# Optimization experiments

Hardware: AMD Instinct MI355X
Metric: run time of the kernel (lower is better)

## Reference

```python
import jax, jax.numpy as jnp
import numpy as np
from jax.ops import segment_sum, segment_max

N_NODES = 50000
N_EDGES = 640000
N_GRAPHS = 128
IN_DIM = 128
HID = 128
OUT_DIM = 2


def setup_inputs() -> dict:
    key = jax.random.key(0)
    ks = jax.random.split(key, 16)
    x = jax.random.normal(ks[0], (N_NODES, IN_DIM), dtype=jnp.float32)
    edge_index = jax.random.randint(ks[1], (2, N_EDGES), 0, N_NODES, dtype=jnp.int64)
    batch = jnp.sort(jax.random.randint(ks[2], (N_NODES,), 0, N_GRAPHS, dtype=jnp.int64))
    s = 0.05
    return {
        "x": x,
        "edge_index": edge_index,
        "batch": batch,
        "w0": jax.random.normal(ks[3], (HID, IN_DIM), dtype=jnp.float32) * s,
        "b0": jnp.zeros((HID,), jnp.float32),
        "w1": jax.random.normal(ks[4], (HID, HID), dtype=jnp.float32) * s,
        "b1": jnp.zeros((HID,), jnp.float32),
        "w2": jax.random.normal(ks[5], (HID, HID), dtype=jnp.float32) * s,
        "b2": jnp.zeros((HID,), jnp.float32),
        "gate_w": jax.random.normal(ks[6], (1, HID), dtype=jnp.float32) * s,
        "gate_b": jnp.zeros((1,), jnp.float32),
        "lin_w": jax.random.normal(ks[7], (2 * HID, HID), dtype=jnp.float32) * s,
        "lin_b": jnp.zeros((2 * HID,), jnp.float32),
        "cls_w": jax.random.normal(ks[8], (OUT_DIM, 2 * HID), dtype=jnp.float32) * s,
        "cls_b": jnp.zeros((OUT_DIM,), jnp.float32),
    }


def _gcn_norm(edge_index, n):
    # add self loops, symmetric normalization D^-1/2 (A+I) D^-1/2
    loop = jnp.arange(n, dtype=edge_index.dtype)
    row = jnp.concatenate([edge_index[0], loop])
    col = jnp.concatenate([edge_index[1], loop])
    deg = segment_sum(jnp.ones_like(col, dtype=jnp.float32), col, num_segments=n)
    dis = jnp.where(deg > 0, jax.lax.rsqrt(deg), 0.0)
    norm = dis[row] * dis[col]
    return row, col, norm


def _gcn_conv(x, w, b, row, col, norm, n):
    xw = x @ w.T + b                     # [N, hid]
    msg = norm[:, None] * xw[row]        # gather + scale, [E+N, hid]
    return segment_sum(msg, col, num_segments=n)


def _att_pool(x, gate_w, gate_b, batch, g):
    gate = x @ gate_w.T + gate_b         # [N, 1]
    m = segment_max(gate, batch, num_segments=g)        # [G, 1]
    e = jnp.exp(gate - m[batch])
    s = segment_sum(e, batch, num_segments=g)           # [G, 1]
    alpha = e / s[batch]                                # [N, 1]
    return segment_sum(alpha * x, batch, num_segments=g)  # [G, hid]


def reference(x, edge_index, batch, w0, b0, w1, b1, w2, b2,
              gate_w, gate_b, lin_w, lin_b, cls_w, cls_b):
    n = N_NODES
    g = N_GRAPHS
    row, col, norm = _gcn_norm(edge_index, n)
    hg = None
    for w, b in ((w0, b0), (w1, b1), (w2, b2)):
        x = _gcn_conv(x, w, b, row, col, norm, n)
        x = jax.nn.relu(x)  # dropout is identity in eval mode
        pooled = _att_pool(x, gate_w, gate_b, batch, g)
        hg = pooled if hg is None else hg + pooled
    out = jax.nn.relu(hg @ lin_w.T + lin_b)
    return out @ cls_w.T + cls_b
```

## Files before the change

kernel.cpp:

```cpp
#include <hip/hip_runtime.h>
#include <hip/hip_bf16.h>
#include <float.h>

#define N_NODES  50000
#define N_EDGES  640000
#define N_GRAPHS 128
#define DIM      128
#define CAP      64
#define ZROW     N_NODES
#define NSLICE   8
#define SLICE_W  6250
#define NCHUNK   256
#define CHUNK_E  2500

typedef __attribute__((ext_vector_type(8))) short bf16x8;
typedef __attribute__((ext_vector_type(4))) float f32x4;

__device__ __forceinline__ unsigned short f2bf(float f){
  unsigned int u = __float_as_uint(f);
  u += 0x7fffu + ((u >> 16) & 1u);
  return (unsigned short)(u >> 16);
}
__device__ __forceinline__ float bf2f(unsigned short h){
  return __uint_as_float(((unsigned int)h) << 16);
}
__device__ __forceinline__ float2 up2(unsigned int p){
  return make_float2(__uint_as_float(p << 16),
                     __uint_as_float(p & 0xffff0000u));
}

__global__ __launch_bounds__(256) void zero_misc(int* __restrict__ cnt,
    unsigned int* __restrict__ z0, unsigned int* __restrict__ z1){
  int i = blockIdx.x*256 + threadIdx.x;
  if (i < N_NODES) cnt[i] = 0;
  else if (i < N_NODES + 64) z0[i - N_NODES] = 0;
  else if (i < N_NODES + 128) z1[i - N_NODES - 64] = 0;
}

__global__ __launch_bounds__(256) void scatter_sliced(
    const int* __restrict__ ei, int* __restrict__ cnt, int* __restrict__ srcb){
  int slice = blockIdx.x & (NSLICE-1);
  int chunk = blockIdx.x >> 3;
  int e0 = chunk * CHUNK_E;
  for (int e = e0 + threadIdx.x; e < e0 + CHUNK_E; e += 256){
    int c = ei[N_EDGES + e];
    if (c / SLICE_W == slice){
      int r = ei[e];
      int pos = atomicAdd(&cnt[c], 1);
      srcb[(c << 6) + pos] = r;
    }
  }
}

__global__ __launch_bounds__(256) void prep(
    const int* __restrict__ cnt, float* __restrict__ dis,
    const int* __restrict__ batch, int* __restrict__ gs,
    const float* __restrict__ w0, const float* __restrict__ w1,
    const float* __restrict__ w2, unsigned int* __restrict__ o0,
    unsigned int* __restrict__ o1, unsigned int* __restrict__ o2){
  int b = blockIdx.x, tid = threadIdx.x;
  if (b < 196){
    int i = b*256 + tid;
    if (i < N_NODES){
      dis[i] = 1.0f / sqrtf((float)(cnt[i] + 1));
      int bb = batch[i];
      int bp = (i == 0) ? -1 : batch[i-1];
      for (int g = bp + 1; g <= bb; ++g) gs[g] = i;
      if (i == N_NODES - 1)
        for (int g = bb + 1; g <= N_GRAPHS; ++g) gs[g] = N_NODES;
    }
  } else {
    int i = (b - 196)*256 + tid;
    if (i < 3*8192){
      int a = i >> 13, j = i & 8191;
      const float* src = (a == 0) ? w0 : (a == 1) ? w1 : w2;
      unsigned int* dst = (a == 0) ? o0 : (a == 1) ? o1 : o2;
      float2 v = ((const float2*)src)[j];
      dst[j] = (unsigned int)f2bf(v.x) | ((unsigned int)f2bf(v.y) << 16);
    }
  }
}

template<bool F32IN>
__global__ __launch_bounds__(256, 2) void gemm_mfma(
    const void* __restrict__ Ain, const unsigned short* __restrict__ Wb,
    const float* __restrict__ bias, const float* __restrict__ dis,
    unsigned short* __restrict__ C, int total_waves){
  int tid = threadIdx.x;
  int lane = tid & 63;
  int wid = blockIdx.x*4 + (tid >> 6);
  int l15 = lane & 15, l4 = lane >> 4;
  bf16x8 wf[8][4];
  #pragma unroll
  for (int ob = 0; ob < 8; ++ob)
    #pragma unroll
    for (int ks = 0; ks < 4; ++ks)
      wf[ob][ks] = *(const bf16x8*)&Wb[(ob*16 + l15)*128 + ks*32 + l4*8];
  float bv[8];
  #pragma unroll
  for (int ob = 0; ob < 8; ++ob) bv[ob] = bias[ob*16 + l15];

  for (int t = wid; t < N_NODES/16; t += total_waves){
    int row0 = t*16;
    bf16x8 af[4];
    #pragma unroll
    for (int ks = 0; ks < 4; ++ks){
      if constexpr (F32IN){
        const float* A = (const float*)Ain;
        const float4* ap = (const float4*)&A[(size_t)(row0 + l15)*128 + ks*32 + l4*8];
        float4 fa = ap[0], fb = ap[1];
        bf16x8 v;
        v[0]=(short)f2bf(fa.x); v[1]=(short)f2bf(fa.y);
        v[2]=(short)f2bf(fa.z); v[3]=(short)f2bf(fa.w);
        v[4]=(short)f2bf(fb.x); v[5]=(short)f2bf(fb.y);
        v[6]=(short)f2bf(fb.z); v[7]=(short)f2bf(fb.w);
        af[ks] = v;
      } else {
        const unsigned short* A = (const unsigned short*)Ain;
        af[ks] = *(const bf16x8*)&A[(size_t)(row0 + l15)*128 + ks*32 + l4*8];
      }
    }
    f32x4 acc[8];
    #pragma unroll
    for (int ob = 0; ob < 8; ++ob) acc[ob] = (f32x4){0.f,0.f,0.f,0.f};
    #pragma unroll
    for (int ks = 0; ks < 4; ++ks)
      #pragma unroll
      for (int ob = 0; ob < 8; ++ob)
        acc[ob] = __builtin_amdgcn_mfma_f32_16x16x32_bf16(af[ks], wf[ob][ks],
                                                          acc[ob], 0, 0, 0);
    float dv[4];
    #pragma unroll
    for (int r = 0; r < 4; ++r) dv[r] = dis[row0 + l4*4 + r];
    #pragma unroll
    for (int ob = 0; ob < 8; ++ob)
      #pragma unroll
      for (int r = 0; r < 4; ++r)
        C[(size_t)(row0 + l4*4 + r)*128 + ob*16 + l15] =
            f2bf((acc[ob][r] + bv[ob]) * dv[r]);
  }
}

__global__ __launch_bounds__(256) void aggregate_bf(
    const uint4* __restrict__ xw4,
    const int* __restrict__ cnt, const int* __restrict__ srcb,
    const float* __restrict__ dis,
    uint4* __restrict__ xout4, const float* __restrict__ gw,
    const float* __restrict__ gb, float* __restrict__ gate){
  int tid  = threadIdx.x;
  int lane = tid & 63;
  int wv   = tid >> 6;
  int quad = wv >> 1;
  int par  = wv & 1;
  int sub  = lane >> 4, l16 = lane & 15;
  int node = blockIdx.x*8 + quad*4 + sub;
  int   n  = cnt[node];
  int base = node << 6;
  float acc[8];
  if (par == 0){
    uint4 v = xw4[node*16 + l16];
    float2 a0 = up2(v.x), a1 = up2(v.y), a2 = up2(v.z), a3 = up2(v.w);
    acc[0]=a0.x; acc[1]=a0.y; acc[2]=a1.x; acc[3]=a1.y;
    acc[4]=a2.x; acc[5]=a2.y; acc[6]=a3.x; acc[7]=a3.y;
  } else {
    #pragma unroll
    for (int i = 0; i < 8; ++i) acc[i] = 0.f;
  }
  int nmax = n;
  nmax = max(nmax, __shfl_xor(nmax, 16, 64));
  nmax = max(nmax, __shfl_xor(nmax, 32, 64));
  for (int e = par*8; e < nmax; e += 16){
    int4 sa = *(const int4*)&srcb[base + e];
    int4 sb = *(const int4*)&srcb[base + e + 4];
    int r0 = (e   < n) ? sa.x : ZROW;
    int r1 = (e+1 < n) ? sa.y : ZROW;
    int r2 = (e+2 < n) ? sa.z : ZROW;
    int r3 = (e+3 < n) ? sa.w : ZROW;
    int r4 = (e+4 < n) ? sb.x : ZROW;
    int r5 = (e+5 < n) ? sb.y : ZROW;
    int r6 = (e+6 < n) ? sb.z : ZROW;
    int r7 = (e+7 < n) ? sb.w : ZROW;
    uint4 u0 = xw4[r0*16 + l16];
    uint4 u1 = xw4[r1*16 + l16];
    uint4 u2 = xw4[r2*16 + l16];
    uint4 u3 = xw4[r3*16 + l16];
    uint4 u4 = xw4[r4*16 + l16];
    uint4 u5 = xw4[r5*16 + l16];
    uint4 u6 = xw4[r6*16 + l16];
    uint4 u7 = xw4[r7*16 + l16];
    #define ACC8(U) { \
      float2 b0=up2(U.x), b1=up2(U.y), b2=up2(U.z), b3=up2(U.w); \
      acc[0]+=b0.x; acc[1]+=b0.y; acc[2]+=b1.x; acc[3]+=b1.y;    \
      acc[4]+=b2.x; acc[5]+=b2.y; acc[6]+=b3.x; acc[7]+=b3.y; }
    ACC8(u0) ACC8(u1) ACC8(u2) ACC8(u3)
    ACC8(u4) ACC8(u5) ACC8(u6) ACC8(u7)
    #undef ACC8
  }
  __shared__ float comb[2][64][9];
  if (par == 1){
    #pragma unroll
    for (int i = 0; i < 8; ++i) comb[quad][lane][i] = acc[i];
  }
  __syncthreads();
  if (par == 0){
    float d = dis[node];
    #pragma unroll
    for (int i = 0; i < 8; ++i)
      acc[i] = fmaxf(d*(acc[i] + comb[quad][lane][i]), 0.f);
    uint4 o;
    o.x = (unsigned int)f2bf(acc[0]) | ((unsigned int)f2bf(acc[1]) << 16);
    o.y = (unsigned int)f2bf(acc[2]) | ((unsigned int)f2bf(acc[3]) << 16);
    o.z = (unsigned int)f2bf(acc[4]) | ((unsigned int)f2bf(acc[5]) << 16);
    o.w = (unsigned int)f2bf(acc[6]) | ((unsigned int)f2bf(acc[7]) << 16);
    xout4[node*16 + l16] = o;
    const float4* gw4 = (const float4*)gw;
    float4 g0 = gw4[l16*2], g1 = gw4[l16*2 + 1];
    float p = acc[0]*g0.x + acc[1]*g0.y + acc[2]*g0.z + acc[3]*g0.w
            + acc[4]*g1.x + acc[5]*g1.y + acc[6]*g1.z + acc[7]*g1.w;
    p += __shfl_xor(p, 1, 64);
    p += __shfl_xor(p, 2, 64);
    p += __shfl_xor(p, 4, 64);
    p += __shfl_xor(p, 8, 64);
    if (l16 == 0) gate[node] = p + gb[0];
  }
}

__global__ __launch_bounds__(256) void gate_reduce(float* __restrict__ gate,
    const int* __restrict__ gs){
  int g = blockIdx.x, tid = threadIdx.x;
  int s = gs[g], e = gs[g+1];
  __shared__ float red[256];
  float m = -FLT_MAX;
  for (int i = s + tid; i < e; i += 256) m = fmaxf(m, gate[i]);
  red[tid] = m; __syncthreads();
  for (int st = 128; st > 0; st >>= 1){
    if (tid < st) red[tid] = fmaxf(red[tid], red[tid+st]);
    __syncthreads();
  }
  m = red[0]; __syncthreads();
  float p = 0.f;
  for (int i = s + tid; i < e; i += 256){
    float ev = __expf(gate[i] - m);
    gate[i] = ev;
    p += ev;
  }
  red[tid] = p; __syncthreads();
  for (int st = 128; st > 0; st >>= 1){
    if (tid < st) red[tid] += red[tid+st];
    __syncthreads();
  }
  float inv = (red[0] > 0.f) ? 1.0f/red[0] : 0.f;
  for (int i = s + tid; i < e; i += 256) gate[i] *= inv;
}

__global__ __launch_bounds__(256) void att_pool_part(
    const unsigned int* __restrict__ x, const float* __restrict__ alpha,
    const int* __restrict__ gs, float* __restrict__ hgp){
  int g = blockIdx.x >> 3, q = blockIdx.x & 7, tid = threadIdx.x;
  int s = gs[g], e = gs[g+1];
  int d2 = tid & 63, rg = tid >> 6;
  float ax = 0.f, ay = 0.f;
  for (int i = s + q*4 + rg; i < e; i += 32){
    float a = alpha[i];
    float2 u = up2(x[(size_t)i*64 + d2]);
    ax += a*u.x; ay += a*u.y;
  }
  __shared__ float2 red[4][64];
  red[rg][d2] = make_float2(ax, ay);
  __syncthreads();
  if (tid < 64){
    float2 r0 = red[0][tid], r1 = red[1][tid], r2 = red[2][tid], r3 = red[3][tid];
    hgp[(size_t)blockIdx.x*128 + 2*tid    ] = r0.x + r1.x + r2.x + r3.x;
    hgp[(size_t)blockIdx.x*128 + 2*tid + 1] = r0.y + r1.y + r2.y + r3.y;
  }
}

__global__ __launch_bounds__(256) void head(const float* __restrict__ hgp,
    const float* __restrict__ lw, const float* __restrict__ lb,
    const float* __restrict__ cw, const float* __restrict__ cb,
    float* __restrict__ out){
  int g = blockIdx.x, tid = threadIdx.x;
  __shared__ float h[128];
  __shared__ float t1[256];
  __shared__ float red[256];
  if (tid < 128){
    float hv = 0.f;
    #pragma unroll
    for (int L = 0; L < 3; ++L){
      const float* hb = hgp + (size_t)(L*8*N_GRAPHS + 8*g)*128;
      #pragma unroll
      for (int q = 0; q < 8; ++q) hv += hb[q*128 + tid];
    }
    h[tid] = hv;
  }
  __syncthreads();
  const float* wr = lw + tid*128;
  float a = 0.f;
  for (int k = 0; k < 128; ++k) a += h[k]*wr[k];
  a = fmaxf(a + lb[tid], 0.f);
  t1[tid] = a;
  __syncthreads();
  int o = tid >> 7, j = tid & 127;
  float p = t1[j]*cw[o*256 + j] + t1[j+128]*cw[o*256 + j + 128];
  red[tid] = p; __syncthreads();
  for (int st = 64; st > 0; st >>= 1){
    if (j < st) red[tid] += red[tid+st];
    __syncthreads();
  }
  if (j == 0) out[g*2 + o] = red[tid] + cb[o];
}

extern "C" void kernel_launch(void* const* d_in, const int* in_sizes, int n_in,
                              void* d_out, int out_size, void* d_ws, size_t ws_size,
                              hipStream_t stream){
  const float* x   = (const float*)d_in[0];
  const int*   ei  = (const int*)d_in[1];
  const int* batch = (const int*)d_in[2];
  const float* w0  = (const float*)d_in[3];
  const float* b0  = (const float*)d_in[4];
  const float* w1  = (const float*)d_in[5];
  const float* b1  = (const float*)d_in[6];
  const float* w2  = (const float*)d_in[7];
  const float* b2  = (const float*)d_in[8];
  const float* gw  = (const float*)d_in[9];
  const float* gb  = (const float*)d_in[10];
  const float* lw  = (const float*)d_in[11];
  const float* lb  = (const float*)d_in[12];
  const float* cw  = (const float*)d_in[13];
  const float* cb  = (const float*)d_in[14];
  float* out = (float*)d_out;
  (void)in_sizes; (void)n_in; (void)out_size; (void)ws_size;

  char* ws = (char*)d_ws;
  size_t off = 0;
  auto alloc = [&](size_t bytes)->char*{
    char* p = ws + off;
    off = (off + bytes + 255) & ~(size_t)255;
    return p;
  };
  float* dis    = (float*)alloc((size_t)N_NODES*4);
  unsigned int* xw   = (unsigned int*)alloc((size_t)(N_NODES+1)*64*4);
  unsigned int* xbuf = (unsigned int*)alloc((size_t)(N_NODES+1)*64*4);
  unsigned int* Wb0  = (unsigned int*)alloc((size_t)DIM*64*4);
  unsigned int* Wb1  = (unsigned int*)alloc((size_t)DIM*64*4);
  unsigned int* Wb2  = (unsigned int*)alloc((size_t)DIM*64*4);
  float* gate  = (float*)alloc((size_t)N_NODES*4);
  float* hgp   = (float*)alloc((size_t)3*8*N_GRAPHS*DIM*4);
  int*   gs    = (int*)alloc((size_t)(N_GRAPHS+1)*4);
  int*   cnt   = (int*)alloc((size_t)N_NODES*4);
  int*   srcb  = (int*)alloc(((size_t)N_NODES*CAP + 64)*4);

  const int T = 256;
  zero_misc     <<<(N_NODES+128+T-1)/T, T, 0, stream>>>(cnt,
                    xw + (size_t)ZROW*64, xbuf + (size_t)ZROW*64);
  scatter_sliced<<<NCHUNK*NSLICE, T, 0, stream>>>(ei, cnt, srcb);
  prep          <<<196 + 96, T, 0, stream>>>(cnt, dis, batch, gs,
                                             w0, w1, w2, Wb0, Wb1, Wb2);

  const unsigned int* Ws[3] = {Wb0, Wb1, Wb2};
  const float* Bs[3] = {b0, b1, b2};
  const void* xin = (const void*)x;
  const int GEMM_BLKS = 512;
  for (int L = 0; L < 3; ++L){
    if (L == 0)
      gemm_mfma<true><<<GEMM_BLKS, 256, 0, stream>>>(
          xin, (const unsigned short*)Ws[L], Bs[L], dis,
          (unsigned short*)xw, GEMM_BLKS*4);
    else
      gemm_mfma<false><<<GEMM_BLKS, 256, 0, stream>>>(
          xin, (const unsigned short*)Ws[L], Bs[L], dis,
          (unsigned short*)xw, GEMM_BLKS*4);
    aggregate_bf<<<N_NODES/8, 256, 0, stream>>>((const uint4*)xw, cnt, srcb,
                                                dis, (uint4*)xbuf, gw, gb, gate);
    gate_reduce <<<N_GRAPHS, 256, 0, stream>>>(gate, gs);
    att_pool_part<<<8*N_GRAPHS, 256, 0, stream>>>(xbuf, gate, gs,
                                                  hgp + (size_t)L*8*N_GRAPHS*DIM);
    xin = (const void*)xbuf;
  }
  head<<<N_GRAPHS, 256, 0, stream>>>(hgp, lw, lb, cw, cb, out);
}
```

Baseline: 202.3 us.

## Fuse attention pooling with next-layer GEMM and defer softmax normalization

New measurement: 198.7 us. About the same (-1.8%).

```diff
diff --git a/kernel.cpp b/kernel.cpp
--- a/kernel.cpp
+++ b/kernel.cpp
@@ -12,6 +12,9 @@
 #define SLICE_W  6250
 #define NCHUNK   256
 #define CHUNK_E  2500
+#define GEMM_BLKS 512
+#define POOL_BLKS 1024
+#define AGG_BLKS  (8*782)
 
 typedef __attribute__((ext_vector_type(8))) short bf16x8;
 typedef __attribute__((ext_vector_type(4))) float f32x4;
@@ -20,9 +23,6 @@
   unsigned int u = __float_as_uint(f);
   u += 0x7fffu + ((u >> 16) & 1u);
   return (unsigned short)(u >> 16);
-}
-__device__ __forceinline__ float bf2f(unsigned short h){
-  return __uint_as_float(((unsigned int)h) << 16);
 }
 __device__ __forceinline__ float2 up2(unsigned int p){
   return make_float2(__uint_as_float(p << 16),
@@ -81,14 +81,11 @@
   }
 }
 
-template<bool F32IN>
-__global__ __launch_bounds__(256, 2) void gemm_mfma(
-    const void* __restrict__ Ain, const unsigned short* __restrict__ Wb,
+__device__ __forceinline__ void gemm_body_bf(int wid,
+    const unsigned short* __restrict__ A, const unsigned short* __restrict__ Wb,
     const float* __restrict__ bias, const float* __restrict__ dis,
     unsigned short* __restrict__ C, int total_waves){
-  int tid = threadIdx.x;
-  int lane = tid & 63;
-  int wid = blockIdx.x*4 + (tid >> 6);
+  int lane = threadIdx.x & 63;
   int l15 = lane & 15, l4 = lane >> 4;
   bf16x8 wf[8][4];
   #pragma unroll
@@ -99,27 +96,12 @@
   float bv[8];
   #pragma unroll
   for (int ob = 0; ob < 8; ++ob) bv[ob] = bias[ob*16 + l15];
-
   for (int t = wid; t < N_NODES/16; t += total_waves){
     int row0 = t*16;
     bf16x8 af[4];
     #pragma unroll
-    for (int ks = 0; ks < 4; ++ks){
-      if constexpr (F32IN){
-        const float* A = (const float*)Ain;
-        const float4* ap = (const float4*)&A[(size_t)(row0 + l15)*128 + ks*32 + l4*8];
-        float4 fa = ap[0], fb = ap[1];
-        bf16x8 v;
-        v[0]=(short)f2bf(fa.x); v[1]=(short)f2bf(fa.y);
-        v[2]=(short)f2bf(fa.z); v[3]=(short)f2bf(fa.w);
-        v[4]=(short)f2bf(fb.x); v[5]=(short)f2bf(fb.y);
-        v[6]=(short)f2bf(fb.z); v[7]=(short)f2bf(fb.w);
-        af[ks] = v;
-      } else {
-        const unsigned short* A = (const unsigned short*)Ain;
-        af[ks] = *(const bf16x8*)&A[(size_t)(row0 + l15)*128 + ks*32 + l4*8];
-      }
-    }
+    for (int ks = 0; ks < 4; ++ks)
+      af[ks] = *(const bf16x8*)&A[(size_t)(row0 + l15)*128 + ks*32 + l4*8];
     f32x4 acc[8];
     #pragma unroll
     for (int ob = 0; ob < 8; ++ob) acc[ob] = (f32x4){0.f,0.f,0.f,0.f};
@@ -139,6 +121,120 @@
         C[(size_t)(row0 + l4*4 + r)*128 + ob*16 + l15] =
             f2bf((acc[ob][r] + bv[ob]) * dv[r]);
   }
+}
+
+__global__ __launch_bounds__(256, 2) void gemm_f32(
+    const float* __restrict__ A, const unsigned short* __restrict__ Wb,
+    const float* __restrict__ bias, const float* __restrict__ dis,
+    unsigned short* __restrict__ C, int total_waves){
+  int lane = threadIdx.x & 63;
+  int wid = blockIdx.x*4 + (threadIdx.x >> 6);
+  int l15 = lane & 15, l4 = lane >> 4;
+  bf16x8 wf[8][4];
+  #pragma unroll
+  for (int ob = 0; ob < 8; ++ob)
+    #pragma unroll
+    for (int ks = 0; ks < 4; ++ks)
+      wf[ob][ks] = *(const bf16x8*)&Wb[(ob*16 + l15)*128 + ks*32 + l4*8];
+  float bv[8];
+  #pragma unroll
+  for (int ob = 0; ob < 8; ++ob) bv[ob] = bias[ob*16 + l15];
+  for (int t = wid; t < N_NODES/16; t += total_waves){
+    int row0 = t*16;
+    bf16x8 af[4];
+    #pragma unroll
+    for (int ks = 0; ks < 4; ++ks){
+      const float4* ap = (const float4*)&A[(size_t)(row0 + l15)*128 + ks*32 + l4*8];
+      float4 fa = ap[0], fb = ap[1];
+      bf16x8 v;
+      v[0]=(short)f2bf(fa.x); v[1]=(short)f2bf(fa.y);
+      v[2]=(short)f2bf(fa.z); v[3]=(short)f2bf(fa.w);
+      v[4]=(short)f2bf(fb.x); v[5]=(short)f2bf(fb.y);
+      v[6]=(short)f2bf(fb.z); v[7]=(short)f2bf(fb.w);
+      af[ks] = v;
+    }
+    f32x4 acc[8];
+    #pragma unroll
+    for (int ob = 0; ob < 8; ++ob) acc[ob] = (f32x4){0.f,0.f,0.f,0.f};
+    #pragma unroll
+    for (int ks = 0; ks < 4; ++ks)
+      #pragma unroll
+      for (int ob = 0; ob < 8; ++ob)
+        acc[ob] = __builtin_amdgcn_mfma_f32_16x16x32_bf16(af[ks], wf[ob][ks],
+                                                          acc[ob], 0, 0, 0);
+    float dv[4];
+    #pragma unroll
+    for (int r = 0; r < 4; ++r) dv[r] = dis[row0 + l4*4 + r];
+    #pragma unroll
+    for (int ob = 0; ob < 8; ++ob)
+      #pragma unroll
+      for (int r = 0; r < 4; ++r)
+        C[(size_t)(row0 + l4*4 + r)*128 + ob*16 + l15] =
+            f2bf((acc[ob][r] + bv[ob]) * dv[r]);
+  }
+}
+
+__device__ __forceinline__ void pool_body(int pbid,
+    const unsigned int* __restrict__ x, const float* __restrict__ gate,
+    const int* __restrict__ gs, float* __restrict__ hgp,
+    float* __restrict__ ssum){
+  int g = pbid >> 3, q = pbid & 7, tid = threadIdx.x;
+  int s = gs[g], e = gs[g+1];
+  __shared__ float red[256];
+  __shared__ float2 red2[4][64];
+  float m = -FLT_MAX;
+  for (int i = s + tid; i < e; i += 256) m = fmaxf(m, gate[i]);
+  red[tid] = m; __syncthreads();
+  for (int st = 128; st > 0; st >>= 1){
+    if (tid < st) red[tid] = fmaxf(red[tid], red[tid+st]);
+    __syncthreads();
+  }
+  m = red[0]; __syncthreads();
+  float p = 0.f;
+  for (int i = s + tid; i < e; i += 256) p += __expf(gate[i] - m);
+  red[tid] = p; __syncthreads();
+  for (int st = 128; st > 0; st >>= 1){
+    if (tid < st) red[tid] += red[tid+st];
+    __syncthreads();
+  }
+  if (tid == 0 && q == 0) ssum[g] = red[0];
+  int d2 = tid & 63, rg = tid >> 6;
+  float ax = 0.f, ay = 0.f;
+  for (int i = s + q*4 + rg; i < e; i += 32){
+    float a = __expf(gate[i] - m);
+    float2 u = up2(x[(size_t)i*64 + d2]);
+    ax += a*u.x; ay += a*u.y;
+  }
+  red2[rg][d2] = make_float2(ax, ay);
+  __syncthreads();
+  if (tid < 64){
+    float2 r0 = red2[0][tid], r1 = red2[1][tid],
+           r2 = red2[2][tid], r3 = red2[3][tid];
+    hgp[(size_t)pbid*128 + 2*tid    ] = r0.x + r1.x + r2.x + r3.x;
+    hgp[(size_t)pbid*128 + 2*tid + 1] = r0.y + r1.y + r2.y + r3.y;
+  }
+}
+
+__global__ __launch_bounds__(256, 2) void pool_gemm(
+    const unsigned int* __restrict__ xb, const float* __restrict__ gate,
+    const int* __restrict__ gs, float* __restrict__ hgp,
+    float* __restrict__ ssum,
+    const unsigned short* __restrict__ Wb, const float* __restrict__ bias,
+    const float* __restrict__ dis, unsigned short* __restrict__ xwout){
+  if (blockIdx.x < GEMM_BLKS){
+    int wid = blockIdx.x*4 + (threadIdx.x >> 6);
+    gemm_body_bf(wid, (const unsigned short*)xb, Wb, bias, dis, xwout,
+                 GEMM_BLKS*4);
+  } else {
+    pool_body(blockIdx.x - GEMM_BLKS, xb, gate, gs, hgp, ssum);
+  }
+}
+
+__global__ __launch_bounds__(256) void att_pool(
+    const unsigned int* __restrict__ xb, const float* __restrict__ gate,
+    const int* __restrict__ gs, float* __restrict__ hgp,
+    float* __restrict__ ssum){
+  pool_body(blockIdx.x, xb, gate, gs, hgp, ssum);
 }
 
 __global__ __launch_bounds__(256) void aggregate_bf(
@@ -153,23 +249,22 @@
   int quad = wv >> 1;
   int par  = wv & 1;
   int sub  = lane >> 4, l16 = lane & 15;
-  int node = blockIdx.x*8 + quad*4 + sub;
-  int   n  = cnt[node];
-  int base = node << 6;
+  int slice = blockIdx.x & 7, within = blockIdx.x >> 3;
+  int loc   = within*8 + quad*4 + sub;
+  bool valid = loc < SLICE_W;
+  int node  = slice*SLICE_W + (valid ? loc : SLICE_W-1);
+  int n     = valid ? cnt[node] : 0;
+  int base  = node << 6;
   float acc[8];
-  if (par == 0){
+  #pragma unroll
+  for (int i = 0; i < 8; ++i) acc[i] = 0.f;
+  if (par == 0 && valid){
     uint4 v = xw4[node*16 + l16];
     float2 a0 = up2(v.x), a1 = up2(v.y), a2 = up2(v.z), a3 = up2(v.w);
     acc[0]=a0.x; acc[1]=a0.y; acc[2]=a1.x; acc[3]=a1.y;
     acc[4]=a2.x; acc[5]=a2.y; acc[6]=a3.x; acc[7]=a3.y;
-  } else {
-    #pragma unroll
-    for (int i = 0; i < 8; ++i) acc[i] = 0.f;
-  }
-  int nmax = n;
-  nmax = max(nmax, __shfl_xor(nmax, 16, 64));
-  nmax = max(nmax, __shfl_xor(nmax, 32, 64));
-  for (int e = par*8; e < nmax; e += 16){
+  }
+  for (int e = par*8; e < n; e += 16){
     int4 sa = *(const int4*)&srcb[base + e];
     int4 sb = *(const int4*)&srcb[base + e + 4];
     int r0 = (e   < n) ? sa.x : ZROW;
@@ -202,7 +297,7 @@
     for (int i = 0; i < 8; ++i) comb[quad][lane][i] = acc[i];
   }
   __syncthreads();
-  if (par == 0){
+  if (par == 0 && valid){
     float d = dis[node];
     #pragma unroll
     for (int i = 0; i < 8; ++i)
@@ -225,57 +320,8 @@
   }
 }
 
-__global__ __launch_bounds__(256) void gate_reduce(float* __restrict__ gate,
-    const int* __restrict__ gs){
-  int g = blockIdx.x, tid = threadIdx.x;
-  int s = gs[g], e = gs[g+1];
-  __shared__ float red[256];
-  float m = -FLT_MAX;
-  for (int i = s + tid; i < e; i += 256) m = fmaxf(m, gate[i]);
-  red[tid] = m; __syncthreads();
-  for (int st = 128; st > 0; st >>= 1){
-    if (tid < st) red[tid] = fmaxf(red[tid], red[tid+st]);
-    __syncthreads();
-  }
-  m = red[0]; __syncthreads();
-  float p = 0.f;
-  for (int i = s + tid; i < e; i += 256){
-    float ev = __expf(gate[i] - m);
-    gate[i] = ev;
-    p += ev;
-  }
-  red[tid] = p; __syncthreads();
-  for (int st = 128; st > 0; st >>= 1){
-    if (tid < st) red[tid] += red[tid+st];
-    __syncthreads();
-  }
-  float inv = (red[0] > 0.f) ? 1.0f/red[0] : 0.f;
-  for (int i = s + tid; i < e; i += 256) gate[i] *= inv;
-}
-
-__global__ __launch_bounds__(256) void att_pool_part(
-    const unsigned int* __restrict__ x, const float* __restrict__ alpha,
-    const int* __restrict__ gs, float* __restrict__ hgp){
-  int g = blockIdx.x >> 3, q = blockIdx.x & 7, tid = threadIdx.x;
-  int s = gs[g], e = gs[g+1];
-  int d2 = tid & 63, rg = tid >> 6;
-  float ax = 0.f, ay = 0.f;
-  for (int i = s + q*4 + rg; i < e; i += 32){
-    float a = alpha[i];
-    float2 u = up2(x[(size_t)i*64 + d2]);
-    ax += a*u.x; ay += a*u.y;
-  }
-  __shared__ float2 red[4][64];
-  red[rg][d2] = make_float2(ax, ay);
-  __syncthreads();
-  if (tid < 64){
-    float2 r0 = red[0][tid], r1 = red[1][tid], r2 = red[2][tid], r3 = red[3][tid];
-    hgp[(size_t)blockIdx.x*128 + 2*tid    ] = r0.x + r1.x + r2.x + r3.x;
-    hgp[(size_t)blockIdx.x*128 + 2*tid + 1] = r0.y + r1.y + r2.y + r3.y;
-  }
-}
-
 __global__ __launch_bounds__(256) void head(const float* __restrict__ hgp,
+    const float* __restrict__ ssum,
     const float* __restrict__ lw, const float* __restrict__ lb,
     const float* __restrict__ cw, const float* __restrict__ cb,
     float* __restrict__ out){
@@ -287,9 +333,12 @@
     float hv = 0.f;
     #pragma unroll
     for (int L = 0; L < 3; ++L){
-      const float* hb = hgp + (size_t)(L*8*N_GRAPHS + 8*g)*128;
+      const float* hb = hgp + (size_t)(L*POOL_BLKS + 8*g)*128;
+      float pp = 0.f;
       #pragma unroll
-      for (int q = 0; q < 8; ++q) hv += hb[q*128 + tid];
+      for (int q = 0; q < 8; ++q) pp += hb[q*128 + tid];
+      float sv = ssum[L*N_GRAPHS + g];
+      hv += (sv > 0.f) ? pp/sv : 0.f;
     }
     h[tid] = hv;
   }
@@ -345,7 +394,8 @@
   unsigned int* Wb1  = (unsigned int*)alloc((size_t)DIM*64*4);
   unsigned int* Wb2  = (unsigned int*)alloc((size_t)DIM*64*4);
   float* gate  = (float*)alloc((size_t)N_NODES*4);
-  float* hgp   = (float*)alloc((size_t)3*8*N_GRAPHS*DIM*4);
+  float* hgp   = (float*)alloc((size_t)3*POOL_BLKS*DIM*4);
+  float* ssum  = (float*)alloc((size_t)3*N_GRAPHS*4);
   int*   gs    = (int*)alloc((size_t)(N_GRAPHS+1)*4);
   int*   cnt   = (int*)alloc((size_t)N_NODES*4);
   int*   srcb  = (int*)alloc(((size_t)N_NODES*CAP + 64)*4);
@@ -357,25 +407,22 @@
   prep          <<<196 + 96, T, 0, stream>>>(cnt, dis, batch, gs,
                                              w0, w1, w2, Wb0, Wb1, Wb2);
 
-  const unsigned int* Ws[3] = {Wb0, Wb1, Wb2};
-  const float* Bs[3] = {b0, b1, b2};
-  const void* xin = (const void*)x;
-  const int GEMM_BLKS = 512;
-  for (int L = 0; L < 3; ++L){
-    if (L == 0)
-      gemm_mfma<true><<<GEMM_BLKS, 256, 0, stream>>>(
-          xin, (const unsigned short*)Ws[L], Bs[L], dis,
-          (unsigned short*)xw, GEMM_BLKS*4);
-    else
-      gemm_mfma<false><<<GEMM_BLKS, 256, 0, stream>>>(
-          xin, (const unsigned short*)Ws[L], Bs[L], dis,
-          (unsigned short*)xw, GEMM_BLKS*4);
-    aggregate_bf<<<N_NODES/8, 256, 0, stream>>>((const uint4*)xw, cnt, srcb,
-                                                dis, (uint4*)xbuf, gw, gb, gate);
-    gate_reduce <<<N_GRAPHS, 256, 0, stream>>>(gate, gs);
-    att_pool_part<<<8*N_GRAPHS, 256, 0, stream>>>(xbuf, gate, gs,
-                                                  hgp + (size_t)L*8*N_GRAPHS*DIM);
-    xin = (const void*)xbuf;
-  }
-  head<<<N_GRAPHS, 256, 0, stream>>>(hgp, lw, lb, cw, cb, out);
-}
+  gemm_f32<<<GEMM_BLKS, 256, 0, stream>>>(x, (const unsigned short*)Wb0, b0,
+                                          dis, (unsigned short*)xw, GEMM_BLKS*4);
+  aggregate_bf<<<AGG_BLKS, 256, 0, stream>>>((const uint4*)xw, cnt, srcb, dis,
+                                             (uint4*)xbuf, gw, gb, gate);
+  pool_gemm<<<GEMM_BLKS + POOL_BLKS, 256, 0, stream>>>(
+      xbuf, gate, gs, hgp, ssum,
+      (const unsigned short*)Wb1, b1, dis, (unsigned short*)xw);
+  aggregate_bf<<<AGG_BLKS, 256, 0, stream>>>((const uint4*)xw, cnt, srcb, dis,
+                                             (uint4*)xbuf, gw, gb, gate);
+  pool_gemm<<<GEMM_BLKS + POOL_BLKS, 256, 0, stream>>>(
+      xbuf, gate, gs, hgp + (size_t)POOL_BLKS*DIM, ssum + N_GRAPHS,
+      (const unsigned short*)Wb2, b2, dis, (unsigned short*)xw);
+  aggregate_bf<<<AGG_BLKS, 256, 0, stream>>>((const uint4*)xw, cnt, srcb, dis,
+                                             (uint4*)xbuf, gw, gb, gate);
+  att_pool<<<POOL_BLKS, 256, 0, stream>>>(xbuf, gate, gs,
+                                          hgp + (size_t)2*POOL_BLKS*DIM,
+                                          ssum + 2*N_GRAPHS);
+  head<<<N_GRAPHS, 256, 0, stream>>>(hgp, ssum, lw, lb, cw, cb, out);
+}
```
